# Optimization experiments

Measured on AMD Instinct MI355X. Metric: run time of the kernel, lower is better.

The kernel has to match this reference:

```python
import jax, jax.numpy as jnp
import numpy as np

T, B, L, E, H = 64, 128, 64, 256, 32  # time steps, envs, tokens, d_model, rnn_h
N = T * B


def setup_inputs() -> dict:
    key = jax.random.key(0)
    ks = jax.random.split(key, 8)
    x = jax.random.normal(ks[0], (N, L, E), dtype=jnp.float32)
    done = jax.random.randint(ks[1], (N,), 0, 2).astype(jnp.float32)
    obs_mask = jax.random.randint(ks[2], (N, L), 0, 2).astype(bool)
    obs_mask = obs_mask.at[:, 0].set(True)  # ensure >=1 attendable token per row
    h0 = jnp.zeros((1, B, H), jnp.float32)
    c0 = jnp.zeros((1, B, H), jnp.float32)
    s = 1.0 / np.sqrt(E)
    in_proj_w = jax.random.normal(ks[3], (3 * E, E), jnp.float32) * s
    out_proj_w = jax.random.normal(ks[4], (E, E), jnp.float32) * s
    w_ih = jax.random.normal(ks[5], (4 * H, E), jnp.float32) * s
    w_hh = jax.random.normal(ks[6], (4 * H, H), jnp.float32) * (1.0 / np.sqrt(H))
    b_ih = jnp.zeros((4 * H,), jnp.float32)
    b_hh = jnp.zeros((4 * H,), jnp.float32)
    critic_w = jax.random.normal(ks[7], (1, H), jnp.float32) * 0.05
    critic_b = jnp.zeros((1,), jnp.float32)
    return dict(x=x, done=done, obs_mask=obs_mask, h0=h0, c0=c0,
                in_proj_w=in_proj_w, out_proj_w=out_proj_w,
                w_ih=w_ih, w_hh=w_hh, b_ih=b_ih, b_hh=b_hh,
                critic_w=critic_w, critic_b=critic_b)


def reference(x, done, obs_mask, h0, c0, in_proj_w, out_proj_w,
              w_ih, w_hh, b_ih, b_hh, critic_w, critic_b):
    # --- single-head MHA with custom boolean mask (torch: True = blocked) ---
    qkv = jnp.einsum('nle,fe->nlf', x, in_proj_w)  # [N, L, 3E]
    q, k, v = jnp.split(qkv, 3, axis=-1)
    scores = jnp.einsum('nqe,nke->nqk', q, k) / jnp.sqrt(jnp.asarray(E, x.dtype))
    # torch code: m = 1 - mask; attn_mask = bool(outer(m, m)) -> blocked where
    # both tokens have obs_mask == 0
    dropped = ~obs_mask  # [N, L]
    blocked = dropped[:, :, None] & dropped[:, None, :]  # [N, L, L]
    scores = jnp.where(blocked, jnp.asarray(-1e9, scores.dtype), scores)
    probs = jax.nn.softmax(scores, axis=-1)
    attn = jnp.einsum('nqk,nke->nqe', probs, v)
    out = jnp.einsum('nle,fe->nlf', attn, out_proj_w)  # out_proj (no bias)
    hidden = out.sum(axis=1)  # sum over tokens -> [N, E]

    # --- per-step LSTM with done-based state reset, as a scan over T ---
    hidden_seq = hidden.reshape(T, B, E)
    done_seq = done.reshape(T, B)

    def step(carry, inp):
        h, c = carry
        xt, dt = inp
        keep = (1.0 - dt)[:, None]  # reset state where episode ended
        h = h * keep
        c = c * keep
        gates = xt @ w_ih.T + h @ w_hh.T + (b_ih + b_hh)  # [B, 4H]
        i, f, g, o = jnp.split(gates, 4, axis=-1)  # torch gate order i,f,g,o
        i = jax.nn.sigmoid(i)
        f = jax.nn.sigmoid(f)
        g = jnp.tanh(g)
        o = jax.nn.sigmoid(o)
        c = f * c + i * g
        h = o * jnp.tanh(c)
        return (h, c), h

    (_, _), hs = jax.lax.scan(step, (h0[0], c0[0]), (hidden_seq, done_seq))
    hid = hs.reshape(N, H)
    value = hid @ critic_w.T + critic_b  # [N, 1]
    return value
```

## Files before the change

### kernel.cpp

```cpp
#include <hip/hip_runtime.h>
#include <math.h>

#define T_STEPS 64
#define B_ENVS 128
#define L_TOK 64
#define E_DIM 256
#define H_DIM 32
#define N_SEQ (T_STEPS * B_ENVS)
#define G4H 128

#define BSTRIDE 264

typedef __bf16 bf16x8 __attribute__((ext_vector_type(8)));
typedef __bf16 bf16x4 __attribute__((ext_vector_type(4)));
typedef float f32x4 __attribute__((ext_vector_type(4)));

__global__ void k_precompute_M(const float* __restrict__ ipw, __bf16* __restrict__ Mtb) {
    const int e = blockIdx.x;
    const int f = threadIdx.x;
    float acc = 0.f;
    for (int c = 0; c < E_DIM; ++c) {
        acc = fmaf(ipw[c * E_DIM + e], ipw[(E_DIM + c) * E_DIM + f], acc);
    }
    Mtb[f * E_DIM + e] = (__bf16)(acc * (1.0f / 16.0f));
}

__global__ void k_precompute_R(const float* __restrict__ w_ih,
                               const float* __restrict__ opw,
                               float* __restrict__ R) {
    const int g = blockIdx.x;
    const int e = threadIdx.x;
    float acc = 0.f;
    for (int ep = 0; ep < E_DIM; ++ep) {
        acc = fmaf(w_ih[g * E_DIM + ep], opw[ep * E_DIM + e], acc);
    }
    R[g * E_DIM + e] = acc;
}

__global__ void k_precompute_Q(const float* __restrict__ ipw,
                               const float* __restrict__ R,
                               float* __restrict__ Q) {
    const int g = blockIdx.x;
    const int i = threadIdx.x;
    float acc = 0.f;
    for (int e = 0; e < E_DIM; ++e) {
        acc = fmaf(ipw[(2 * E_DIM + e) * E_DIM + i], R[g * E_DIM + e], acc);
    }
    Q[i * G4H + g] = acc;
}

__global__ __launch_bounds__(1024, 8) void k_attn(const float* __restrict__ x,
                                                  const int* __restrict__ obs_mask,
                                                  const __bf16* __restrict__ Mtb,
                                                  const float* __restrict__ Q,
                                                  float* __restrict__ gates_x) {
    __shared__ __align__(16) __bf16 xb[L_TOK * BSTRIDE];
    __shared__ __align__(16) __bf16 ybuf[L_TOK * BSTRIDE];
    __shared__ float dropped[64];
    __shared__ float pcol[4][64];

    float* upart = (float*)ybuf;
    float* u_l   = (float*)ybuf + 1024;
    float* gpart = (float*)ybuf + 1280;

    const int n = blockIdx.x;
    const int t = threadIdx.x;
    const int lane = t & 63;
    const int w = t >> 6;
    const int lane15 = lane & 15;
    const int quad = lane >> 4;
    const float* xn = x + (size_t)n * (L_TOK * E_DIM);

    if (t < 64) dropped[t] = (obs_mask[n * L_TOK + t] == 0) ? 1.0f : 0.0f;

    {
        const float4* x4 = (const float4*)xn;
#pragma unroll
        for (int it = 0; it < 4; ++it) {
            const int flat4 = t + 1024 * it;
            const int row = flat4 >> 6;
            const int col = (flat4 & 63) * 4;
            const float4 v = x4[flat4];
            bf16x4 pk;
            pk.x = (__bf16)v.x; pk.y = (__bf16)v.y;
            pk.z = (__bf16)v.z; pk.w = (__bf16)v.w;
            *(bf16x4*)&xb[row * BSTRIDE + col] = pk;
        }
    }
    __syncthreads();

    {
        f32x4 acc1[4];
#pragma unroll
        for (int rt = 0; rt < 4; ++rt) acc1[rt] = (f32x4)0.f;

        const __bf16* mrow = Mtb + (size_t)(16 * w + lane15) * E_DIM;
#pragma unroll 2
        for (int kc = 0; kc < 8; ++kc) {
            const int kofs = kc * 32 + quad * 8;
            const bf16x8 bfrag = *(const bf16x8*)(mrow + kofs);
#pragma unroll
            for (int rt = 0; rt < 4; ++rt) {
                const bf16x8 afrag = *(const bf16x8*)&xb[(16 * rt + lane15) * BSTRIDE + kofs];
                acc1[rt] = __builtin_amdgcn_mfma_f32_16x16x32_bf16(afrag, bfrag, acc1[rt], 0, 0, 0);
            }
        }
#pragma unroll
        for (int rt = 0; rt < 4; ++rt) {
            const int col = 16 * w + lane15;
#pragma unroll
            for (int r = 0; r < 4; ++r)
                ybuf[(16 * rt + 4 * quad + r) * BSTRIDE + col] = (__bf16)acc1[rt][r];
        }
    }
    __syncthreads();

    if (w < 4) {
        f32x4 acc2[4];
#pragma unroll
        for (int ct = 0; ct < 4; ++ct) acc2[ct] = (f32x4)0.f;
#pragma unroll 2
        for (int kc = 0; kc < 8; ++kc) {
            const int kofs = kc * 32 + quad * 8;
            const bf16x8 a2 = *(const bf16x8*)&ybuf[(16 * w + lane15) * BSTRIDE + kofs];
#pragma unroll
            for (int ct = 0; ct < 4; ++ct) {
                const bf16x8 b2 = *(const bf16x8*)&xb[(16 * ct + lane15) * BSTRIDE + kofs];
                acc2[ct] = __builtin_amdgcn_mfma_f32_16x16x32_bf16(a2, b2, acc2[ct], 0, 0, 0);
            }
        }
        float db[4];
#pragma unroll
        for (int ct = 0; ct < 4; ++ct) db[ct] = dropped[16 * ct + lane15];
        float colpart[4] = {0.f, 0.f, 0.f, 0.f};
#pragma unroll
        for (int r = 0; r < 4; ++r) {
            const float da = dropped[16 * w + 4 * quad + r];
            float s[4];
#pragma unroll
            for (int ct = 0; ct < 4; ++ct) {
                s[ct] = acc2[ct][r];
                if (da > 0.5f && db[ct] > 0.5f) s[ct] = -1e9f;
            }
            float mx = fmaxf(fmaxf(s[0], s[1]), fmaxf(s[2], s[3]));
#pragma unroll
            for (int off = 1; off < 16; off <<= 1) mx = fmaxf(mx, __shfl_xor(mx, off));
            float p[4], ssum = 0.f;
#pragma unroll
            for (int ct = 0; ct < 4; ++ct) { p[ct] = __expf(s[ct] - mx); ssum += p[ct]; }
#pragma unroll
            for (int off = 1; off < 16; off <<= 1) ssum += __shfl_xor(ssum, off);
            const float inv = 1.0f / ssum;
#pragma unroll
            for (int ct = 0; ct < 4; ++ct) colpart[ct] = fmaf(p[ct], inv, colpart[ct]);
        }
#pragma unroll
        for (int ct = 0; ct < 4; ++ct) {
            float cp = colpart[ct];
            cp += __shfl_xor(cp, 16);
            cp += __shfl_xor(cp, 32);
            colpart[ct] = cp;
        }
        if (quad == 0) {
#pragma unroll
            for (int ct = 0; ct < 4; ++ct) pcol[w][16 * ct + lane15] = colpart[ct];
        }
    }
    __syncthreads();

    if (t < 64) dropped[t] = pcol[0][t] + pcol[1][t] + pcol[2][t] + pcol[3][t];
    __syncthreads();

    {
        const int i = t & 255;
        const int kg = t >> 8;
        float acc = 0.f;
#pragma unroll
        for (int k = 16 * kg; k < 16 * kg + 16; ++k) {
            acc = fmaf(dropped[k], (float)xb[k * BSTRIDE + i], acc);
        }
        upart[kg * 256 + i] = acc;
    }
    __syncthreads();
    if (t < 256)
        u_l[t] = upart[t] + upart[256 + t] + upart[512 + t] + upart[768 + t];
    __syncthreads();

    {
        const int g = t & 127;
        const int q = t >> 7;
        float acc = 0.f;
#pragma unroll
        for (int i = 32 * q; i < 32 * q + 32; ++i)
            acc = fmaf(u_l[i], Q[i * G4H + g], acc);
        gpart[q * 128 + g] = acc;
    }
    __syncthreads();
    if (t < 128) {
        float gx = 0.f;
#pragma unroll
        for (int q = 0; q < 8; ++q) gx += gpart[q * 128 + t];
        gates_x[(size_t)n * G4H + t] = gx;
    }
}

__device__ __forceinline__ float sigmoidf_(float v) {
    return 1.0f / (1.0f + __expf(-v));
}
__device__ __forceinline__ float tanh_safe(float v) {
    const float av = fabsf(v);
    const float e = __expf(-2.0f * av);
    const float r = (1.0f - e) / (1.0f + e);
    return v < 0.f ? -r : r;
}

__global__ __launch_bounds__(64) void k_lstm(const float* __restrict__ gates_x,
                                             const float* __restrict__ done,
                                             const float* __restrict__ h0,
                                             const float* __restrict__ c0,
                                             const float* __restrict__ w_hh,
                                             const float* __restrict__ b_ih,
                                             const float* __restrict__ b_hh,
                                             const float* __restrict__ critic_w,
                                             const float* __restrict__ critic_b,
                                             float* __restrict__ out) {
    const int b = blockIdx.x;
    const int l = threadIdx.x;
    const int g0 = l;
    const int g1 = 64 + l;

    float wr0[H_DIM], wr1[H_DIM];
#pragma unroll
    for (int k = 0; k < H_DIM; ++k) {
        wr0[k] = w_hh[g0 * H_DIM + k];
        wr1[k] = w_hh[g1 * H_DIM + k];
    }
    const float bs0 = b_ih[g0] + b_hh[g0];
    const float bs1 = b_ih[g1] + b_hh[g1];

    float h_reg = (l < H_DIM) ? h0[b * H_DIM + l] : 0.f;
    float c_reg = (l < H_DIM) ? c0[b * H_DIM + l] : 0.f;
    const float cw = (l < H_DIM) ? critic_w[l] : 0.f;
    const float cb = critic_b[0];

    float nx0 = gates_x[(size_t)b * G4H + g0];
    float nx1 = gates_x[(size_t)b * G4H + g1];
    float nd  = done[b];

    for (int step = 0; step < T_STEPS; ++step) {
        const float gx0 = nx0, gx1 = nx1, dv = nd;
        const int ns = (step + 1 < T_STEPS) ? step + 1 : step;
        const size_t nb = (size_t)(ns * B_ENVS + b) * G4H;
        nx0 = gates_x[nb + g0];
        nx1 = gates_x[nb + g1];
        nd  = done[ns * B_ENVS + b];

        const float keep = 1.0f - dv;
        float d0 = 0.f, d1 = 0.f;
#pragma unroll
        for (int k = 0; k < H_DIM; ++k) {
            const float hk = __shfl(h_reg, k);
            d0 = fmaf(hk, wr0[k], d0);
            d1 = fmaf(hk, wr1[k], d1);
        }
        const float pre0 = gx0 + bs0 + keep * d0;
        const float pre1 = gx1 + bs1 + keep * d1;

        const float act0 = sigmoidf_(pre0);
        const float act1 = (l < 32) ? tanh_safe(pre1)
                                    : sigmoidf_(pre1);
        const float fv = __shfl_xor(act0, 32);
        const float ov = __shfl_xor(act1, 32);

        c_reg = fmaf(fv, keep * c_reg, act0 * act1);
        h_reg = ov * tanh_safe(c_reg);
        float val = h_reg * cw;
#pragma unroll
        for (int off = 1; off < 32; off <<= 1) val += __shfl_xor(val, off);
        if (l == 0) out[step * B_ENVS + b] = val + cb;
    }
}

extern "C" void kernel_launch(void* const* d_in, const int* in_sizes, int n_in,
                              void* d_out, int out_size, void* d_ws, size_t ws_size,
                              hipStream_t stream) {
    const float* x    = (const float*)d_in[0];
    const float* done = (const float*)d_in[1];
    const int* mask   = (const int*)d_in[2];
    const float* h0   = (const float*)d_in[3];
    const float* c0   = (const float*)d_in[4];
    const float* ipw  = (const float*)d_in[5];
    const float* opw  = (const float*)d_in[6];
    const float* w_ih = (const float*)d_in[7];
    const float* w_hh = (const float*)d_in[8];
    const float* b_ih = (const float*)d_in[9];
    const float* b_hh = (const float*)d_in[10];
    const float* cw   = (const float*)d_in[11];
    const float* cb   = (const float*)d_in[12];
    float* out = (float*)d_out;

    char* ws = (char*)d_ws;
    __bf16* Mtb = (__bf16*)(ws);
    float* R    = (float*)(ws + (128 * 1024));
    float* Q    = (float*)(ws + (256 * 1024));
    float* gx   = (float*)(ws + (384 * 1024));

    k_precompute_M<<<256, 256, 0, stream>>>(ipw, Mtb);
    k_precompute_R<<<128, 256, 0, stream>>>(w_ih, opw, R);
    k_precompute_Q<<<128, 256, 0, stream>>>(ipw, R, Q);
    k_attn<<<N_SEQ, 1024, 0, stream>>>(x, mask, Mtb, Q, gx);
    k_lstm<<<B_ENVS, 64, 0, stream>>>(gx, done, h0, c0, w_hh, b_ih, b_hh, cw, cb, out);
}
```

Measured before the change: 902.7 us.

## Spread attention score MFMA and softmax across all 16 waves

New measurement: 922.4 us. 1.02x slower.

```diff
diff --git a/kernel.cpp b/kernel.cpp
--- a/kernel.cpp
+++ b/kernel.cpp
@@ -57,7 +57,8 @@
     __shared__ __align__(16) __bf16 xb[L_TOK * BSTRIDE];
     __shared__ __align__(16) __bf16 ybuf[L_TOK * BSTRIDE];
     __shared__ float dropped[64];
-    __shared__ float pcol[4][64];
+    __shared__ float rowpart[4][64];
+    __shared__ float pcolpart[4][64];
 
     float* upart = (float*)ybuf;
     float* u_l   = (float*)ybuf + 1024;
@@ -115,60 +116,46 @@
     }
     __syncthreads();
 
-    if (w < 4) {
-        f32x4 acc2[4];
-#pragma unroll
-        for (int ct = 0; ct < 4; ++ct) acc2[ct] = (f32x4)0.f;
-#pragma unroll 2
+    {
+        const int rg = w >> 2;
+        const int cg = w & 3;
+
+        f32x4 acc2 = (f32x4)0.f;
+#pragma unroll
         for (int kc = 0; kc < 8; ++kc) {
             const int kofs = kc * 32 + quad * 8;
-            const bf16x8 a2 = *(const bf16x8*)&ybuf[(16 * w + lane15) * BSTRIDE + kofs];
-#pragma unroll
-            for (int ct = 0; ct < 4; ++ct) {
-                const bf16x8 b2 = *(const bf16x8*)&xb[(16 * ct + lane15) * BSTRIDE + kofs];
-                acc2[ct] = __builtin_amdgcn_mfma_f32_16x16x32_bf16(a2, b2, acc2[ct], 0, 0, 0);
-            }
-        }
-        float db[4];
-#pragma unroll
-        for (int ct = 0; ct < 4; ++ct) db[ct] = dropped[16 * ct + lane15];
-        float colpart[4] = {0.f, 0.f, 0.f, 0.f};
+            const bf16x8 a2 = *(const bf16x8*)&ybuf[(16 * rg + lane15) * BSTRIDE + kofs];
+            const bf16x8 b2 = *(const bf16x8*)&xb[(16 * cg + lane15) * BSTRIDE + kofs];
+            acc2 = __builtin_amdgcn_mfma_f32_16x16x32_bf16(a2, b2, acc2, 0, 0, 0);
+        }
+        const float db = dropped[16 * cg + lane15];
+        float e4[4];
 #pragma unroll
         for (int r = 0; r < 4; ++r) {
-            const float da = dropped[16 * w + 4 * quad + r];
-            float s[4];
-#pragma unroll
-            for (int ct = 0; ct < 4; ++ct) {
-                s[ct] = acc2[ct][r];
-                if (da > 0.5f && db[ct] > 0.5f) s[ct] = -1e9f;
-            }
-            float mx = fmaxf(fmaxf(s[0], s[1]), fmaxf(s[2], s[3]));
-#pragma unroll
-            for (int off = 1; off < 16; off <<= 1) mx = fmaxf(mx, __shfl_xor(mx, off));
-            float p[4], ssum = 0.f;
-#pragma unroll
-            for (int ct = 0; ct < 4; ++ct) { p[ct] = __expf(s[ct] - mx); ssum += p[ct]; }
-#pragma unroll
-            for (int off = 1; off < 16; off <<= 1) ssum += __shfl_xor(ssum, off);
-            const float inv = 1.0f / ssum;
-#pragma unroll
-            for (int ct = 0; ct < 4; ++ct) colpart[ct] = fmaf(p[ct], inv, colpart[ct]);
-        }
-#pragma unroll
-        for (int ct = 0; ct < 4; ++ct) {
-            float cp = colpart[ct];
-            cp += __shfl_xor(cp, 16);
-            cp += __shfl_xor(cp, 32);
-            colpart[ct] = cp;
-        }
-        if (quad == 0) {
-#pragma unroll
-            for (int ct = 0; ct < 4; ++ct) pcol[w][16 * ct + lane15] = colpart[ct];
-        }
-    }
-    __syncthreads();
-
-    if (t < 64) dropped[t] = pcol[0][t] + pcol[1][t] + pcol[2][t] + pcol[3][t];
+            const float da = dropped[16 * rg + 4 * quad + r];
+            e4[r] = (da > 0.5f && db > 0.5f) ? 0.f : __expf(acc2[r]);
+        }
+#pragma unroll
+        for (int r = 0; r < 4; ++r) {
+            float v = e4[r];
+#pragma unroll
+            for (int off = 1; off < 16; off <<= 1) v += __shfl_xor(v, off);
+            if (lane15 == 0) rowpart[cg][16 * rg + 4 * quad + r] = v;
+        }
+        __syncthreads();
+
+        float cp = 0.f;
+#pragma unroll
+        for (int r = 0; r < 4; ++r) {
+            const int R = 16 * rg + 4 * quad + r;
+            const float rsum = rowpart[0][R] + rowpart[1][R] +
+                               rowpart[2][R] + rowpart[3][R];
+            cp = fmaf(e4[r], 1.0f / rsum, cp);
+        }
+        cp += __shfl_xor(cp, 16);
+        cp += __shfl_xor(cp, 32);
+        if (lane < 16) pcolpart[rg][16 * cg + lane15] = cp;
+    }
     __syncthreads();
 
     {
@@ -177,7 +164,9 @@
         float acc = 0.f;
 #pragma unroll
         for (int k = 16 * kg; k < 16 * kg + 16; ++k) {
-            acc = fmaf(dropped[k], (float)xb[k * BSTRIDE + i], acc);
+            const float wk = pcolpart[0][k] + pcolpart[1][k] +
+                             pcolpart[2][k] + pcolpart[3][k];
+            acc = fmaf(wk, (float)xb[k * BSTRIDE + i], acc);
         }
         upart[kg * 256 + i] = acc;
     }
```
